# Optimization experiments

Measured on AMD Instinct MI355X. Metric: run time of the kernel, lower is better.

The kernel has to match this reference:

```python
import jax, jax.numpy as jnp
import numpy as np

B, S, H, NH = 2, 2048, 2048, 16
HD = H // NH  # 128
ROPE_BASE = 10000.0


def _rope(q, k, position_ids):
    # q, k: [B, NH, S, HD]; position_ids: [B, S]
    half = HD // 2
    inv_freq = 1.0 / (ROPE_BASE ** (jnp.arange(0, half, dtype=jnp.float32) / half))
    freqs = position_ids.astype(jnp.float32)[:, :, None] * inv_freq[None, None, :]  # [B,S,half]
    emb = jnp.concatenate([freqs, freqs], axis=-1)                                   # [B,S,HD]
    cos = jnp.cos(emb)[:, None, :, :]  # [B,1,S,HD]
    sin = jnp.sin(emb)[:, None, :, :]

    def rot_half(x):
        x1, x2 = jnp.split(x, 2, axis=-1)
        return jnp.concatenate([-x2, x1], axis=-1)

    q = q * cos + rot_half(q) * sin
    k = k * cos + rot_half(k) * sin
    return q, k


def setup_inputs() -> dict:
    key = jax.random.key(0)
    k1, k2, k3 = jax.random.split(key, 3)
    hidden_states = jax.random.normal(k1, (B, S, H), dtype=jnp.float32)
    position_ids = jnp.broadcast_to(jnp.arange(S, dtype=jnp.int32), (B, S))
    # additive causal mask (large finite negative to avoid inf arithmetic)
    causal = jnp.triu(jnp.full((S, S), -1e9, dtype=jnp.float32), k=1)
    attention_mask = jnp.broadcast_to(causal[None, None], (B, 1, S, S))
    qkv_w = jax.random.normal(k2, (3 * H, H), dtype=jnp.float32) * (H ** -0.5)
    qkv_b = jnp.zeros((3 * H,), dtype=jnp.float32)
    o_w = jax.random.normal(k3, (H, H), dtype=jnp.float32) * (H ** -0.5)
    return {"hidden_states": hidden_states, "position_ids": position_ids,
            "attention_mask": attention_mask, "qkv_w": qkv_w, "qkv_b": qkv_b, "o_w": o_w}


def reference(hidden_states, position_ids, attention_mask, qkv_w, qkv_b, o_w):
    qkv = hidden_states @ qkv_w.T + qkv_b                      # [B,S,3H]
    q, k, v = jnp.split(qkv, 3, axis=-1)

    def to_heads(x):
        return x.reshape(B, S, NH, HD).transpose(0, 2, 1, 3)   # [B,NH,S,HD]

    q, k, v = to_heads(q), to_heads(k), to_heads(v)
    q, k = _rope(q, k, position_ids)

    scale = 1.0 / np.sqrt(HD)
    scores = jnp.einsum('bhqd,bhkd->bhqk', q, k * scale)
    scores = scores + attention_mask
    probs = jax.nn.softmax(scores.astype(jnp.float32), axis=-1).astype(q.dtype)
    attn = jnp.einsum('bhqk,bhkd->bhqd', probs, v)
    attn = attn.transpose(0, 2, 1, 3).reshape(B, S, H)
    return attn @ o_w.T
```

## Files before the change

kernel.cpp:

```cpp
#include <hip/hip_runtime.h>
#include <hip/hip_bf16.h>

#define BB 2
#define SS 2048
#define HH 2048
#define NHH 16
#define HDD 128

using f32x4  = __attribute__((ext_vector_type(4))) float;
using bf16x8 = __attribute__((ext_vector_type(8))) short;

__device__ __forceinline__ unsigned short f2bf(float x) {
  unsigned int u = __float_as_uint(x);
  unsigned int r = (u + 0x7FFFu + ((u >> 16) & 1u)) >> 16;
  return (unsigned short)r;
}
__device__ __forceinline__ float bf2f(unsigned short u) {
  return __uint_as_float(((unsigned int)u) << 16);
}

__device__ __forceinline__ void gll16(const void* g, void* l) {
  __builtin_amdgcn_global_load_lds(
      (__attribute__((address_space(1))) void*)(g),
      (__attribute__((address_space(3))) void*)(l), 16, 0, 0);
}

#define MFMA16(a, b, c) __builtin_amdgcn_mfma_f32_16x16x32_bf16(a, b, c, 0, 0, 0)

template<int N> __device__ __forceinline__ void wlgkm() {
  static_assert(N == 0 || N == 2 || N == 4 || N == 6 || N == 8 || N == 10 || N == 12,
                "unsupported lgkmcnt");
  if constexpr (N == 0)       asm volatile("s_waitcnt lgkmcnt(0)"  ::: "memory");
  else if constexpr (N == 2)  asm volatile("s_waitcnt lgkmcnt(2)"  ::: "memory");
  else if constexpr (N == 4)  asm volatile("s_waitcnt lgkmcnt(4)"  ::: "memory");
  else if constexpr (N == 6)  asm volatile("s_waitcnt lgkmcnt(6)"  ::: "memory");
  else if constexpr (N == 8)  asm volatile("s_waitcnt lgkmcnt(8)"  ::: "memory");
  else if constexpr (N == 10) asm volatile("s_waitcnt lgkmcnt(10)" ::: "memory");
  else if constexpr (N == 12) asm volatile("s_waitcnt lgkmcnt(12)" ::: "memory");
}
template<int N> __device__ __forceinline__ void wvm() {
  static_assert(N == 0 || N == 5 || N == 6 || N == 7 || N == 8, "unsupported vmcnt");
  if constexpr (N == 0)      asm volatile("s_waitcnt vmcnt(0)" ::: "memory");
  else if constexpr (N == 5) asm volatile("s_waitcnt vmcnt(5)" ::: "memory");
  else if constexpr (N == 6) asm volatile("s_waitcnt vmcnt(6)" ::: "memory");
  else if constexpr (N == 7) asm volatile("s_waitcnt vmcnt(7)" ::: "memory");
  else if constexpr (N == 8) asm volatile("s_waitcnt vmcnt(8)" ::: "memory");
}


__global__ void convert_bf16(const float* __restrict__ in, unsigned short* __restrict__ out, int n4) {
  int i = blockIdx.x * blockDim.x + threadIdx.x;
  if (i >= n4) return;
  float4 v = reinterpret_cast<const float4*>(in)[i];
  ushort4 o;
  o.x = f2bf(v.x); o.y = f2bf(v.y); o.z = f2bf(v.z); o.w = f2bf(v.w);
  reinterpret_cast<ushort4*>(out)[i] = o;
}

__global__ void build_tab(float* __restrict__ tab) {
  int i = blockIdx.x * blockDim.x + threadIdx.x;
  if (i >= SS * 64) return;
  int s = i >> 6, j = i & 63;
  float invf = expf(-logf(10000.f) * ((float)j / 64.f));
  float a = (float)s * invf;
  tab[i * 2]     = cosf(a);
  tab[i * 2 + 1] = sinf(a);
}


__global__ __launch_bounds__(512, 1)
void gemm_qkv(const unsigned short* __restrict__ A,
              const unsigned short* __restrict__ Bw,
              const float* __restrict__ bias,
              const int* __restrict__ pos,
              const float* __restrict__ tab,
              unsigned short* __restrict__ outQ,
              unsigned short* __restrict__ outK,
              unsigned short* __restrict__ outV,
              int Kdim) {
  __shared__ unsigned short lds_[4][256 * 64];
  const int tid = threadIdx.x;
  const int tn = blockIdx.x, tm = blockIdx.y;
  const int wid = tid >> 6, lane = tid & 63;
  const int wm = wid >> 2, wn = wid & 3;
  const int lr = lane & 15, lg = lane >> 4;

  const unsigned short* Ab = A + (size_t)tm * 256 * Kdim;
  const unsigned short* Bb = Bw + (size_t)tn * 256 * Kdim;

  f32x4 acc[8][4] = {};
  bf16x8 af[8][2], bfr[4][2];

  const int nt = Kdim >> 6;

  auto stageA = [&](int t, int h) {
    unsigned short* L = lds_[t & 1];
    const int k0 = t << 6;
#pragma unroll
    for (int p = 0; p < 2; ++p) {
      int cl = p * 512 + tid;
      int ri = cl >> 3, c = cl & 7;
      int row = (ri >> 6) * 128 + h * 64 + (ri & 63);
      int cg = c ^ (row & 7);
      gll16(Ab + (size_t)row * Kdim + k0 + (cg << 3), L + row * 64 + (c << 3));
    }
  };
  auto stageB = [&](int t, int h) {
    unsigned short* L = lds_[2 + (t & 1)];
    const int k0 = t << 6;
#pragma unroll
    for (int p = 0; p < 2; ++p) {
      int cl = p * 512 + tid;
      int ri = cl >> 3, c = cl & 7;
      int row = (ri >> 5 << 6) + (h << 5) + (ri & 31);
      int cg = c ^ (row & 7);
      gll16(Bb + (size_t)row * Kdim + k0 + (cg << 3), L + row * 64 + (c << 3));
    }
  };
  auto readAhalf = [&](int g, int h) {
    const unsigned short* la = lds_[g & 1];
#pragma unroll
    for (int mi = h * 4; mi < h * 4 + 4; ++mi) {
      int ra = wm * 128 + mi * 16 + lr;
      af[mi][0] = *reinterpret_cast<const bf16x8*>(la + ra * 64 + ((lg ^ (ra & 7)) << 3));
      af[mi][1] = *reinterpret_cast<const bf16x8*>(la + ra * 64 + (((4 + lg) ^ (ra & 7)) << 3));
    }
  };
  auto readBhalf = [&](int g, int h) {
    const unsigned short* lb = lds_[2 + (g & 1)];
#pragma unroll
    for (int ni = h * 2; ni < h * 2 + 2; ++ni) {
      int rb = wn * 64 + ni * 16 + lr;
      bfr[ni][0] = *reinterpret_cast<const bf16x8*>(lb + rb * 64 + ((lg ^ (rb & 7)) << 3));
      bfr[ni][1] = *reinterpret_cast<const bf16x8*>(lb + rb * 64 + (((4 + lg) ^ (rb & 7)) << 3));
    }
  };
  auto quad = [&](int ah, int bh) {
    __builtin_amdgcn_s_setprio(1);
#pragma unroll
    for (int mi = ah * 4; mi < ah * 4 + 4; ++mi)
#pragma unroll
      for (int ni = bh * 2; ni < bh * 2 + 2; ++ni) {
        acc[mi][ni] = MFMA16(af[mi][0], bfr[ni][0], acc[mi][ni]);
        acc[mi][ni] = MFMA16(af[mi][1], bfr[ni][1], acc[mi][ni]);
      }
    __builtin_amdgcn_s_setprio(0);
  };

  stageA(0, 0); stageA(0, 1); stageB(0, 0); stageB(0, 1);
  stageA(1, 0); stageA(1, 1); stageB(1, 0); stageB(1, 1);
  wvm<8>();
  __builtin_amdgcn_s_barrier();
  __builtin_amdgcn_sched_barrier(0);
  readAhalf(0, 0);
  readBhalf(0, 0);

  for (int g = 0; g < nt; ++g) {
    readBhalf(g, 1);
    wlgkm<4>();
    __builtin_amdgcn_sched_barrier(0);
    quad(0, 0);

    readAhalf(g, 1);
    wlgkm<8>();
    __builtin_amdgcn_sched_barrier(0);
    quad(0, 1);

    asm volatile("s_waitcnt vmcnt(0) lgkmcnt(0)" ::: "memory");
    __builtin_amdgcn_s_barrier();
    __builtin_amdgcn_sched_barrier(0);
    if (g + 1 < nt) readAhalf(g + 1, 0);
    if (g + 2 < nt) { stageA(g + 2, 0); stageA(g + 2, 1); }
    quad(1, 0);

    if (g + 1 < nt) readBhalf(g + 1, 0);
    if (g + 2 < nt) { stageB(g + 2, 0); stageB(g + 2, 1); }
    quad(1, 1);
  }

  if (tn < 16) {
    unsigned short* Ls = &lds_[0][0];
    __syncthreads();
#pragma unroll
    for (int mi = 0; mi < 8; ++mi) {
#pragma unroll
      for (int ni = 0; ni < 4; ++ni) {
        int n_l = wn * 64 + ni * 16 + lr;
        float bv = bias[tn * 256 + n_l];
#pragma unroll
        for (int r = 0; r < 4; ++r) {
          int m_l = wm * 128 + mi * 16 + lg * 4 + r;
          Ls[m_l * 256 + (n_l ^ ((m_l & 7) << 3))] = f2bf(acc[mi][ni][r] + bv);
        }
      }
    }
    __syncthreads();

    unsigned short* outX = (tn < 8) ? outQ : outK;
    const int jb = (tid & 7) * 8;
    const int r0 = (tid >> 3) * 4;
#pragma unroll
    for (int rr = 0; rr < 4; ++rr) {
      int row = r0 + rr;
      int m = tm * 256 + row;
      int b = m >> 11, s = m & 2047;
      int p = pos[b * 2048 + s];
      float cs[8], sn[8];
#pragma unroll
      for (int j = 0; j < 8; ++j) {
        float2 t2 = *reinterpret_cast<const float2*>(&tab[((size_t)p * 64 + jb + j) * 2]);
        cs[j] = t2.x; sn[j] = t2.y;
      }
      int swz = (row & 7) << 3;
#pragma unroll
      for (int hb = 0; hb < 2; ++hb) {
        bf16x8 x1 = *reinterpret_cast<const bf16x8*>(&Ls[row * 256 + (hb * 128 + (jb ^ swz))]);
        bf16x8 x2 = *reinterpret_cast<const bf16x8*>(&Ls[row * 256 + (hb * 128 + 64 + (jb ^ swz))]);
        bf16x8 y1, y2;
#pragma unroll
        for (int j = 0; j < 8; ++j) {
          float a1 = bf2f((unsigned short)x1[j]);
          float a2 = bf2f((unsigned short)x2[j]);
          y1[j] = (short)f2bf(a1 * cs[j] - a2 * sn[j]);
          y2[j] = (short)f2bf(a2 * cs[j] + a1 * sn[j]);
        }
        int n0 = tn * 256 + hb * 128;
        int h = (n0 >> 7) & 15;
        unsigned short* dst = outX + (((size_t)(b * 16 + h)) * 2048 + s) * 128;
        *reinterpret_cast<bf16x8*>(&dst[jb]) = y1;
        *reinterpret_cast<bf16x8*>(&dst[64 + jb]) = y2;
      }
    }
  } else {
#pragma unroll
    for (int mi = 0; mi < 8; ++mi) {
#pragma unroll
      for (int ni = 0; ni < 4; ++ni) {
        int n = tn * 256 + wn * 64 + ni * 16 + lr;
        float bv = bias[n];
        int h = (n >> 7) & 15;
        int d = n & 127;
#pragma unroll
        for (int r = 0; r < 4; ++r) {
          int m = tm * 256 + wm * 128 + mi * 16 + lg * 4 + r;
          int b = m >> 11;
          int s = m & 2047;
          outV[(((size_t)(b * 16 + h)) * 128 + d) * 2048 + s] = f2bf(acc[mi][ni][r] + bv);
        }
      }
    }
  }
}


template<int MODE>
__global__ __launch_bounds__(256)
void gemm97(const unsigned short* __restrict__ A,
            const unsigned short* __restrict__ Bw,
            float* __restrict__ outF,
            int Kdim) {
  __shared__ unsigned short lA[128 * 64];
  __shared__ unsigned short lB[128 * 64];
  const int tid = threadIdx.x;
  const int tn = blockIdx.x, tm = blockIdx.y;
  const int wid = tid >> 6, lane = tid & 63;
  const int wm = wid >> 1, wn = wid & 1;
  const int lr = lane & 15, lg = lane >> 4;

  const unsigned short* Ab = A + (size_t)tm * 128 * Kdim;
  const unsigned short* Bb = Bw + (size_t)tn * 128 * Kdim;

  f32x4 acc[4][4] = {};

  const unsigned short* sa[4];
  const unsigned short* sb[4];
  unsigned short* da[4];
  unsigned short* db[4];
#pragma unroll
  for (int p = 0; p < 4; ++p) {
    int cl = p * 256 + tid;
    int ri = cl >> 3, c = cl & 7;
    int cg = c ^ (ri & 7);
    sa[p] = Ab + (size_t)ri * Kdim + (cg << 3);
    sb[p] = Bb + (size_t)ri * Kdim + (cg << 3);
    da[p] = lA + ri * 64 + (c << 3);
    db[p] = lB + ri * 64 + (c << 3);
  }

  const int nt = Kdim >> 6;

  for (int k = 0; k < nt; ++k) {
#pragma unroll
    for (int p = 0; p < 4; ++p) {
      gll16(sa[p], da[p]); sa[p] += 64;
      gll16(sb[p], db[p]); sb[p] += 64;
    }
    __syncthreads();

    bf16x8 af[4][2], bf[4][2];
#pragma unroll
    for (int t = 0; t < 4; ++t) {
      int ra = wm * 64 + t * 16 + lr;
      int rb = wn * 64 + t * 16 + lr;
      af[t][0] = *reinterpret_cast<const bf16x8*>(lA + ra * 64 + ((lg ^ (ra & 7)) << 3));
      af[t][1] = *reinterpret_cast<const bf16x8*>(lA + ra * 64 + (((4 + lg) ^ (ra & 7)) << 3));
      bf[t][0] = *reinterpret_cast<const bf16x8*>(lB + rb * 64 + ((lg ^ (rb & 7)) << 3));
      bf[t][1] = *reinterpret_cast<const bf16x8*>(lB + rb * 64 + (((4 + lg) ^ (rb & 7)) << 3));
    }
#pragma unroll
    for (int i = 0; i < 4; ++i)
#pragma unroll
      for (int j = 0; j < 4; ++j) {
        acc[i][j] = MFMA16(af[i][0], bf[j][0], acc[i][j]);
        acc[i][j] = MFMA16(af[i][1], bf[j][1], acc[i][j]);
      }
    __syncthreads();
  }

#pragma unroll
  for (int i = 0; i < 4; ++i) {
#pragma unroll
    for (int j = 0; j < 4; ++j) {
      int n = tn * 128 + wn * 64 + j * 16 + lr;
#pragma unroll
      for (int r = 0; r < 4; ++r) {
        int m = tm * 128 + wm * 64 + i * 16 + lg * 4 + r;
        outF[(size_t)m * 2048 + n] = acc[i][j][r];
      }
    }
  }
}


__global__ __launch_bounds__(256)
void attn_fwd(const unsigned short* __restrict__ Qr,
              const unsigned short* __restrict__ Kr,
              const unsigned short* __restrict__ Vt,
              unsigned short* __restrict__ attnb) {
  __shared__ unsigned short Ks[2][64 * 128];
  __shared__ unsigned short Vs[2][128 * 64];
  __shared__ unsigned short Ps[64 * 64];
  const int bx = blockIdx.x, bh = blockIdx.y;
  const int tid = threadIdx.x;
  const int wid = tid >> 6, lane = tid & 63;
  const int lr = lane & 15, lg = lane >> 4;
  const unsigned short* Qb = Qr + (size_t)bh * SS * HDD;
  const unsigned short* Kb = Kr + (size_t)bh * SS * HDD;
  const unsigned short* Vb = Vt + (size_t)bh * HDD * SS;
  const int b = bh >> 4, h = bh & 15;
  const float SC2 = 0.12751763f;

  const unsigned short* ksrc0[4];
  const unsigned short* vsrc0[4];
  int dst8[4];
#pragma unroll
  for (int ch = 0; ch < 4; ++ch) {
    int c = tid + ch * 256;
    int kr = c >> 4, kc = c & 15;
    ksrc0[ch] = Kb + (size_t)kr * 128 + ((kc ^ (kr & 7)) << 3);
    int vr = c >> 3, vc = c & 7;
    vsrc0[ch] = Vb + (size_t)vr * SS + ((vc ^ (vr & 7)) << 3);
    dst8[ch] = c * 8;
  }
  const unsigned short* ksrc[4];
  const unsigned short* vsrc[4];

  auto stage = [&](int buf) {
#pragma unroll
    for (int ch = 0; ch < 4; ++ch) {
      gll16(ksrc[ch], Ks[buf] + dst8[ch]); ksrc[ch] += 64 * 128;
      gll16(vsrc[ch], Vs[buf] + dst8[ch]); vsrc[ch] += 64;
    }
  };

#pragma unroll 1
  for (int qi = 0; qi < 2; ++qi) {
    const int qt = qi ? bx : (31 - bx);

#pragma unroll
    for (int ch = 0; ch < 4; ++ch) { ksrc[ch] = ksrc0[ch]; vsrc[ch] = vsrc0[ch]; }

    bf16x8 qf[4];
#pragma unroll
    for (int kk = 0; kk < 4; ++kk)
      qf[kk] = *reinterpret_cast<const bf16x8*>(
          Qb + ((size_t)(qt * 64 + wid * 16 + lr)) * 128 + kk * 32 + lg * 8);

    f32x4 oacc[8] = {};
    float mrow[4], lsum[4];
#pragma unroll
    for (int r = 0; r < 4; ++r) { mrow[r] = -1e30f; lsum[r] = 0.f; }

    int cur = 0;
    stage(0);

#pragma unroll 1
    for (int kt = 0; kt <= qt; ++kt) {
      if (kt < qt) {
        stage(cur ^ 1);
        asm volatile("s_waitcnt vmcnt(8)" ::: "memory");
      } else {
        asm volatile("s_waitcnt vmcnt(0)" ::: "memory");
      }
      __builtin_amdgcn_s_barrier();
      __builtin_amdgcn_sched_barrier(0);

      float sv[4][4];
#pragma unroll
      for (int nt = 0; nt < 4; ++nt) {
        f32x4 sa = {};
#pragma unroll
        for (int kk = 0; kk < 4; ++kk) {
          int row = nt * 16 + lr;
          bf16x8 kf = *reinterpret_cast<const bf16x8*>(
              Ks[cur] + row * 128 + (((kk * 4 + lg) ^ (row & 7)) << 3));
          sa = __builtin_amdgcn_mfma_f32_16x16x32_bf16(qf[kk], kf, sa, 0, 0, 0);
        }
#pragma unroll
        for (int r = 0; r < 4; ++r) {
          float s = sa[r] * SC2;
          if (kt == qt && (nt * 16 + lr) > (wid * 16 + lg * 4 + r)) s -= 1.5e9f;
          sv[nt][r] = s;
        }
      }

      float tmax[4];
#pragma unroll
      for (int r = 0; r < 4; ++r)
        tmax[r] = fmaxf(fmaxf(sv[0][r], sv[1][r]), fmaxf(sv[2][r], sv[3][r]));
#pragma unroll
      for (int r = 0; r < 4; ++r) {
        tmax[r] = fmaxf(tmax[r], __shfl_xor(tmax[r], 1));
        tmax[r] = fmaxf(tmax[r], __shfl_xor(tmax[r], 2));
        tmax[r] = fmaxf(tmax[r], __shfl_xor(tmax[r], 4));
        tmax[r] = fmaxf(tmax[r], __shfl_xor(tmax[r], 8));
      }

      float need = fmaxf(fmaxf(tmax[0] - mrow[0], tmax[1] - mrow[1]),
                         fmaxf(tmax[2] - mrow[2], tmax[3] - mrow[3]));
      if (__any(need > 11.54f)) {
#pragma unroll
        for (int r = 0; r < 4; ++r) {
          float mn = fmaxf(mrow[r], tmax[r]);
          float fr = exp2f(mrow[r] - mn);
          mrow[r] = mn;
          lsum[r] *= fr;
#pragma unroll
          for (int ct = 0; ct < 8; ++ct) oacc[ct][r] *= fr;
        }
      }

      float tsum[4] = {0.f, 0.f, 0.f, 0.f};
#pragma unroll
      for (int nt = 0; nt < 4; ++nt) {
        int colc = nt * 2 + (lr >> 3);
#pragma unroll
        for (int r = 0; r < 4; ++r) {
          float p = exp2f(sv[nt][r] - mrow[r]);
          tsum[r] += p;
          int row = wid * 16 + lg * 4 + r;
          Ps[row * 64 + ((colc ^ (row & 7)) << 3) + (lr & 7)] = f2bf(p);
        }
      }
#pragma unroll
      for (int r = 0; r < 4; ++r) {
        tsum[r] += __shfl_xor(tsum[r], 1);
        tsum[r] += __shfl_xor(tsum[r], 2);
        tsum[r] += __shfl_xor(tsum[r], 4);
        tsum[r] += __shfl_xor(tsum[r], 8);
        lsum[r] += tsum[r];
      }

      bf16x8 pf[2];
#pragma unroll
      for (int ks = 0; ks < 2; ++ks) {
        int row = wid * 16 + lr;
        pf[ks] = *reinterpret_cast<const bf16x8*>(
            Ps + row * 64 + (((ks * 4 + lg) ^ (row & 7)) << 3));
      }
#pragma unroll
      for (int ct = 0; ct < 8; ++ct) {
#pragma unroll
        for (int ks = 0; ks < 2; ++ks) {
          int row = ct * 16 + lr;
          bf16x8 vf = *reinterpret_cast<const bf16x8*>(
              Vs[cur] + row * 64 + (((ks * 4 + lg) ^ (row & 7)) << 3));
          oacc[ct] = __builtin_amdgcn_mfma_f32_16x16x32_bf16(pf[ks], vf, oacc[ct], 0, 0, 0);
        }
      }
      __builtin_amdgcn_s_barrier();
      cur ^= 1;
    }

#pragma unroll
    for (int r = 0; r < 4; ++r) {
      float rl = 1.f / lsum[r];
      int qg = qt * 64 + wid * 16 + lg * 4 + r;
#pragma unroll
      for (int ct = 0; ct < 8; ++ct) {
        int d = ct * 16 + lr;
        attnb[((size_t)b * SS + qg) * HH + h * 128 + d] = f2bf(oacc[ct][r] * rl);
      }
    }
  }
}


extern "C" void kernel_launch(void* const* d_in, const int* in_sizes, int n_in,
                              void* d_out, int out_size, void* d_ws, size_t ws_size,
                              hipStream_t stream) {
  const float* hs     = (const float*)d_in[0];
  const int*   pos    = (const int*)d_in[1];
  const float* qkv_w  = (const float*)d_in[3];
  const float* qkv_b  = (const float*)d_in[4];
  const float* o_w    = (const float*)d_in[5];
  float* out = (float*)d_out;
  char* ws = (char*)d_ws;

  unsigned short* hsb   = (unsigned short*)(ws);
  unsigned short* wqkvb = (unsigned short*)(ws + 16777216);
  unsigned short* owb   = (unsigned short*)(ws + 41943040);
  unsigned short* Qr    = (unsigned short*)(ws + 50331648);
  unsigned short* Kr    = (unsigned short*)(ws + 67108864);
  unsigned short* Vt    = (unsigned short*)(ws + 83886080);
  unsigned short* attnb = (unsigned short*)(ws + 100663296);
  float*          tab   = (float*)(ws + 117440512);

  convert_bf16<<<2097152 / 256, 256, 0, stream>>>(hs, hsb, 2097152);
  convert_bf16<<<3145728 / 256, 256, 0, stream>>>(qkv_w, wqkvb, 3145728);
  convert_bf16<<<1048576 / 256, 256, 0, stream>>>(o_w, owb, 1048576);
  build_tab<<<512, 256, 0, stream>>>(tab);

  gemm_qkv<<<dim3(24, 16), 512, 0, stream>>>(hsb, wqkvb, qkv_b, pos, tab, Qr, Kr, Vt, 2048);
  attn_fwd<<<dim3(16, 32), 256, 0, stream>>>(Qr, Kr, Vt, attnb);
  gemm97<0><<<dim3(16, 32), 256, 0, stream>>>(attnb, owb, out, 2048);
}
```

Measured before the change: 281.4 us.

## Enlarge attention Q tile to 128 rows with 8 waves; fuse prep kernels

The attention kernel now processes 128-row query tiles with 512 threads (8 waves), so each staged K/V tile in shared memory is reused by twice as many query rows. The grid is halved and the causal loop iterates over 64-wide KV tiles up to 2*qt+2. Separately, the three bf16 conversion launches and the RoPE table build are merged into a single prep kernel to cut launch overhead. The risks are fewer blocks for load balancing and extra masked work on the diagonal tiles, plus higher register pressure under launch_bounds(512,4).

Result: slower. 299.8 us (+6.5%).

```diff
diff --git a/kernel.cpp b/kernel.cpp
--- a/kernel.cpp
+++ b/kernel.cpp
@@ -28,43 +28,41 @@
 #define MFMA16(a, b, c) __builtin_amdgcn_mfma_f32_16x16x32_bf16(a, b, c, 0, 0, 0)
 
 template<int N> __device__ __forceinline__ void wlgkm() {
-  static_assert(N == 0 || N == 2 || N == 4 || N == 6 || N == 8 || N == 10 || N == 12,
-                "unsupported lgkmcnt");
-  if constexpr (N == 0)       asm volatile("s_waitcnt lgkmcnt(0)"  ::: "memory");
-  else if constexpr (N == 2)  asm volatile("s_waitcnt lgkmcnt(2)"  ::: "memory");
-  else if constexpr (N == 4)  asm volatile("s_waitcnt lgkmcnt(4)"  ::: "memory");
-  else if constexpr (N == 6)  asm volatile("s_waitcnt lgkmcnt(6)"  ::: "memory");
-  else if constexpr (N == 8)  asm volatile("s_waitcnt lgkmcnt(8)"  ::: "memory");
-  else if constexpr (N == 10) asm volatile("s_waitcnt lgkmcnt(10)" ::: "memory");
-  else if constexpr (N == 12) asm volatile("s_waitcnt lgkmcnt(12)" ::: "memory");
+  static_assert(N == 0 || N == 4 || N == 8, "unsupported lgkmcnt");
+  if constexpr (N == 0)      asm volatile("s_waitcnt lgkmcnt(0)" ::: "memory");
+  else if constexpr (N == 4) asm volatile("s_waitcnt lgkmcnt(4)" ::: "memory");
+  else if constexpr (N == 8) asm volatile("s_waitcnt lgkmcnt(8)" ::: "memory");
 }
 template<int N> __device__ __forceinline__ void wvm() {
-  static_assert(N == 0 || N == 5 || N == 6 || N == 7 || N == 8, "unsupported vmcnt");
+  static_assert(N == 0 || N == 4 || N == 8, "unsupported vmcnt");
   if constexpr (N == 0)      asm volatile("s_waitcnt vmcnt(0)" ::: "memory");
-  else if constexpr (N == 5) asm volatile("s_waitcnt vmcnt(5)" ::: "memory");
-  else if constexpr (N == 6) asm volatile("s_waitcnt vmcnt(6)" ::: "memory");
-  else if constexpr (N == 7) asm volatile("s_waitcnt vmcnt(7)" ::: "memory");
+  else if constexpr (N == 4) asm volatile("s_waitcnt vmcnt(4)" ::: "memory");
   else if constexpr (N == 8) asm volatile("s_waitcnt vmcnt(8)" ::: "memory");
 }
 
 
-__global__ void convert_bf16(const float* __restrict__ in, unsigned short* __restrict__ out, int n4) {
+__global__ void prep(const float* __restrict__ hs, const float* __restrict__ qkv_w,
+                     const float* __restrict__ o_w, unsigned short* __restrict__ hsb,
+                     unsigned short* __restrict__ wqkvb, unsigned short* __restrict__ owb,
+                     float* __restrict__ tab) {
   int i = blockIdx.x * blockDim.x + threadIdx.x;
-  if (i >= n4) return;
-  float4 v = reinterpret_cast<const float4*>(in)[i];
-  ushort4 o;
-  o.x = f2bf(v.x); o.y = f2bf(v.y); o.z = f2bf(v.z); o.w = f2bf(v.w);
-  reinterpret_cast<ushort4*>(out)[i] = o;
-}
-
-__global__ void build_tab(float* __restrict__ tab) {
-  int i = blockIdx.x * blockDim.x + threadIdx.x;
-  if (i >= SS * 64) return;
-  int s = i >> 6, j = i & 63;
-  float invf = expf(-logf(10000.f) * ((float)j / 64.f));
-  float a = (float)s * invf;
-  tab[i * 2]     = cosf(a);
-  tab[i * 2 + 1] = sinf(a);
+  if (i < 6291456) {
+    const float* src; unsigned short* dst; int j;
+    if (i < 2097152)      { src = hs;    dst = hsb;   j = i; }
+    else if (i < 5242880) { src = qkv_w; dst = wqkvb; j = i - 2097152; }
+    else                  { src = o_w;   dst = owb;   j = i - 5242880; }
+    float4 v = reinterpret_cast<const float4*>(src)[j];
+    ushort4 o;
+    o.x = f2bf(v.x); o.y = f2bf(v.y); o.z = f2bf(v.z); o.w = f2bf(v.w);
+    reinterpret_cast<ushort4*>(dst)[j] = o;
+  } else {
+    int j = i - 6291456;
+    int s = j >> 6, jj = j & 63;
+    float invf = expf(-logf(10000.f) * ((float)jj / 64.f));
+    float a = (float)s * invf;
+    tab[j * 2]     = cosf(a);
+    tab[j * 2 + 1] = sinf(a);
+  }
 }
 
 
@@ -332,14 +330,14 @@
 }
 
 
-__global__ __launch_bounds__(256)
+__global__ __launch_bounds__(512, 4)
 void attn_fwd(const unsigned short* __restrict__ Qr,
               const unsigned short* __restrict__ Kr,
               const unsigned short* __restrict__ Vt,
               unsigned short* __restrict__ attnb) {
   __shared__ unsigned short Ks[2][64 * 128];
   __shared__ unsigned short Vs[2][128 * 64];
-  __shared__ unsigned short Ps[64 * 64];
+  __shared__ unsigned short Ps[128 * 64];
   const int bx = blockIdx.x, bh = blockIdx.y;
   const int tid = threadIdx.x;
   const int wid = tid >> 6, lane = tid & 63;
@@ -350,41 +348,29 @@
   const int b = bh >> 4, h = bh & 15;
   const float SC2 = 0.12751763f;
 
-  const unsigned short* ksrc0[4];
-  const unsigned short* vsrc0[4];
-  int dst8[4];
-#pragma unroll
-  for (int ch = 0; ch < 4; ++ch) {
-    int c = tid + ch * 256;
-    int kr = c >> 4, kc = c & 15;
-    ksrc0[ch] = Kb + (size_t)kr * 128 + ((kc ^ (kr & 7)) << 3);
-    int vr = c >> 3, vc = c & 7;
-    vsrc0[ch] = Vb + (size_t)vr * SS + ((vc ^ (vr & 7)) << 3);
-    dst8[ch] = c * 8;
-  }
-  const unsigned short* ksrc[4];
-  const unsigned short* vsrc[4];
-
-  auto stage = [&](int buf) {
-#pragma unroll
-    for (int ch = 0; ch < 4; ++ch) {
-      gll16(ksrc[ch], Ks[buf] + dst8[ch]); ksrc[ch] += 64 * 128;
-      gll16(vsrc[ch], Vs[buf] + dst8[ch]); vsrc[ch] += 64;
-    }
-  };
-
 #pragma unroll 1
   for (int qi = 0; qi < 2; ++qi) {
-    const int qt = qi ? bx : (31 - bx);
-
-#pragma unroll
-    for (int ch = 0; ch < 4; ++ch) { ksrc[ch] = ksrc0[ch]; vsrc[ch] = vsrc0[ch]; }
+    const int qt = qi ? bx : (15 - bx);
+    const int nkt = 2 * qt + 2;
+
+    const unsigned short* ksrc[2];
+    const unsigned short* vsrc[2];
+    int dst8[2];
+#pragma unroll
+    for (int ch = 0; ch < 2; ++ch) {
+      int c = tid + ch * 512;
+      int kr = c >> 4, kc = c & 15;
+      ksrc[ch] = Kb + (size_t)kr * 128 + ((kc ^ (kr & 7)) << 3);
+      int vr = c >> 3, vc = c & 7;
+      vsrc[ch] = Vb + (size_t)vr * SS + ((vc ^ (vr & 7)) << 3);
+      dst8[ch] = c * 8;
+    }
 
     bf16x8 qf[4];
 #pragma unroll
     for (int kk = 0; kk < 4; ++kk)
       qf[kk] = *reinterpret_cast<const bf16x8*>(
-          Qb + ((size_t)(qt * 64 + wid * 16 + lr)) * 128 + kk * 32 + lg * 8);
+          Qb + ((size_t)(qt * 128 + wid * 16 + lr)) * 128 + kk * 32 + lg * 8);
 
     f32x4 oacc[8] = {};
     float mrow[4], lsum[4];
@@ -392,15 +378,23 @@
     for (int r = 0; r < 4; ++r) { mrow[r] = -1e30f; lsum[r] = 0.f; }
 
     int cur = 0;
-    stage(0);
+#pragma unroll
+    for (int ch = 0; ch < 2; ++ch) {
+      gll16(ksrc[ch], Ks[0] + dst8[ch]); ksrc[ch] += 64 * 128;
+      gll16(vsrc[ch], Vs[0] + dst8[ch]); vsrc[ch] += 64;
+    }
 
 #pragma unroll 1
-    for (int kt = 0; kt <= qt; ++kt) {
-      if (kt < qt) {
-        stage(cur ^ 1);
-        asm volatile("s_waitcnt vmcnt(8)" ::: "memory");
+    for (int kt = 0; kt < nkt; ++kt) {
+      if (kt + 1 < nkt) {
+#pragma unroll
+        for (int ch = 0; ch < 2; ++ch) {
+          gll16(ksrc[ch], Ks[cur ^ 1] + dst8[ch]); ksrc[ch] += 64 * 128;
+          gll16(vsrc[ch], Vs[cur ^ 1] + dst8[ch]); vsrc[ch] += 64;
+        }
+        wvm<4>();
       } else {
-        asm volatile("s_waitcnt vmcnt(0)" ::: "memory");
+        wvm<0>();
       }
       __builtin_amdgcn_s_barrier();
       __builtin_amdgcn_sched_barrier(0);
@@ -419,7 +413,8 @@
 #pragma unroll
         for (int r = 0; r < 4; ++r) {
           float s = sa[r] * SC2;
-          if (kt == qt && (nt * 16 + lr) > (wid * 16 + lg * 4 + r)) s -= 1.5e9f;
+          if ((kt >> 1) == qt &&
+              ((kt & 1) << 6) + nt * 16 + lr > wid * 16 + lg * 4 + r) s -= 1.5e9f;
           sv[nt][r] = s;
         }
       }
@@ -495,7 +490,7 @@
 #pragma unroll
     for (int r = 0; r < 4; ++r) {
       float rl = 1.f / lsum[r];
-      int qg = qt * 64 + wid * 16 + lg * 4 + r;
+      int qg = qt * 128 + wid * 16 + lg * 4 + r;
 #pragma unroll
       for (int ct = 0; ct < 8; ++ct) {
         int d = ct * 16 + lr;
@@ -526,12 +521,9 @@
   unsigned short* attnb = (unsigned short*)(ws + 100663296);
   float*          tab   = (float*)(ws + 117440512);
 
-  convert_bf16<<<2097152 / 256, 256, 0, stream>>>(hs, hsb, 2097152);
-  convert_bf16<<<3145728 / 256, 256, 0, stream>>>(qkv_w, wqkvb, 3145728);
-  convert_bf16<<<1048576 / 256, 256, 0, stream>>>(o_w, owb, 1048576);
-  build_tab<<<512, 256, 0, stream>>>(tab);
+  prep<<<25088, 256, 0, stream>>>(hs, qkv_w, o_w, hsb, wqkvb, owb, tab);
 
   gemm_qkv<<<dim3(24, 16), 512, 0, stream>>>(hsb, wqkvb, qkv_b, pos, tab, Qr, Kr, Vt, 2048);
-  attn_fwd<<<dim3(16, 32), 256, 0, stream>>>(Qr, Kr, Vt, attnb);
+  attn_fwd<<<dim3(8, 32), 512, 0, stream>>>(Qr, Kr, Vt, attnb);
   gemm97<0><<<dim3(16, 32), 256, 0, stream>>>(attnb, owb, out, 2048);
 }
```
